# Performance work log

Measured on AMD Instinct MI355X. Metric: run time of the kernel, lower is better.

The kernel has to match this reference:

```python
import jax, jax.numpy as jnp
import numpy as np

B, KEY, D, U, MODES = 16384, 64, 128, 128, 32

def setup_inputs() -> dict:
    key = jax.random.key(0)
    k1, k2, k3, k4, k5 = jax.random.split(key, 5)
    return {
        "key": jax.random.normal(k1, (B, KEY), dtype=jnp.float32),
        "x": jax.random.normal(k2, (B, D), dtype=jnp.float32),
        "sens": jnp.ones((MODES,), dtype=jnp.float32),
        "keys_map": jax.random.normal(k3, (MODES, KEY), dtype=jnp.float32),
        "kernels": jax.random.normal(k4, (MODES, D, U), dtype=jnp.float32) * 0.05,
        "biases": jax.random.normal(k5, (MODES, U), dtype=jnp.float32) * 0.05,
    }

def reference(key, x, sens, keys_map, kernels, biases):
    # key: [B, KEY]; keys_map: [MODES, KEY]
    # Euclidean distance of each key to each mode's stored key.
    dist = jnp.sqrt(jnp.sum((key[:, None, :] - keys_map[None, :, :]) ** 2, axis=-1))  # [B, MODES]
    sim = jax.nn.softmax(sens / (dist + 1.0), axis=-1)  # [B, MODES]
    modes = kernels.shape[0]
    # Original: kernel_b = mean_m(sim[b,m] * kernels[m]); out_b = x_b @ kernel_b.
    # Reordered as GEMM-per-mode + weighted combine (same math):
    out = jnp.einsum('bm,bd,mdu->bu', sim, x, kernels) / modes  # [B, U]
    out = out + (sim @ biases) / modes  # mean over modes of sim-weighted biases
    return out
```

## Files before the change

### kernel.cpp

```cpp
#include <hip/hip_runtime.h>

#define BATCH 16384
#define KEYD  64
#define DDIM  128
#define UDIM  128
#define MODES 32

typedef __attribute__((ext_vector_type(8))) short bf16x8;
typedef __attribute__((ext_vector_type(4))) float f32x4;

__device__ __forceinline__ unsigned short f2bf(float f) {
  unsigned u = __float_as_uint(f);
  unsigned r = (u + 0x7FFFu + ((u >> 16) & 1u)) >> 16;
  return (unsigned short)r;
}

__device__ __forceinline__ void gld_lds16(const void* g, void* l) {
  __builtin_amdgcn_global_load_lds(
      (const __attribute__((address_space(1))) unsigned int*)g,
      (__attribute__((address_space(3))) unsigned int*)l, 16, 0, 0);
}

__global__ __launch_bounds__(256) void prep_all(
    const float* __restrict__ key, const float* __restrict__ x,
    const float* __restrict__ sens, const float* __restrict__ keys_map,
    const float* __restrict__ kernels, const float* __restrict__ biases,
    float* __restrict__ sim, unsigned short* __restrict__ x16,
    unsigned short* __restrict__ kb16, unsigned short* __restrict__ bb16) {
  const int t = threadIdx.x;
  const int bid = blockIdx.x;

  if (bid < BATCH / 32) {
    __shared__ float kr[32][KEYD];
    *(float4*)(&kr[0][0] + t * 4) =
        *(const float4*)(key + (long)bid * 32 * KEYD + t * 4);
    *(float4*)(&kr[0][0] + 1024 + t * 4) =
        *(const float4*)(key + (long)bid * 32 * KEYD + 1024 + t * 4);

    const int lane = t & 63, wave = t >> 6;
    const int m = lane & 31, h = lane >> 5;
    float kreg[32];
    {
      const float* kmp = keys_map + m * KEYD + h * 32;
      #pragma unroll
      for (int j = 0; j < 32; j += 4) {
        const float4 v = *(const float4*)(kmp + j);
        kreg[j] = v.x; kreg[j + 1] = v.y; kreg[j + 2] = v.z; kreg[j + 3] = v.w;
      }
    }
    const float sv = sens[m];
    __syncthreads();

    #pragma unroll
    for (int rr = 0; rr < 8; ++rr) {
      const int rl = wave * 8 + rr;
      const long row = (long)bid * 32 + rl;

      float d2h = 0.f;
      #pragma unroll
      for (int j = 0; j < 32; j += 2) {
        const float2 kv = *(const float2*)(&kr[rl][h * 32 + j]);
        float a = kv.x - kreg[j], b = kv.y - kreg[j + 1];
        d2h += a * a + b * b;
      }
      float d2 = d2h + __shfl_xor(d2h, 32, 64);
      float logit = sv / (sqrtf(d2) + 1.0f);
      float mx = logit;
      #pragma unroll
      for (int off = 16; off > 0; off >>= 1) mx = fmaxf(mx, __shfl_xor(mx, off, 64));
      float e = __expf(logit - mx);
      float s = e;
      #pragma unroll
      for (int off = 16; off > 0; off >>= 1) s += __shfl_xor(s, off, 64);
      if (h == 0) sim[row * MODES + m] = e / s;

      const float2 xv = *(const float2*)(x + row * DDIM + lane * 2);
      ushort2 o; o.x = f2bf(xv.x); o.y = f2bf(xv.y);
      *(ushort2*)(x16 + row * DDIM + lane * 2) = o;
    }
  } else {
    int tt = (bid - BATCH / 32) * 256 + t;
    if (tt < MODES * 16 * UDIM) {
      int u = tt & 127, kb = (tt >> 7) & 15, m = tt >> 11;
      const float* src = kernels + (long)((m * 16 + kb) * 8) * UDIM + u;
      ushort4 lo, hi;
      lo.x = f2bf(src[0 * UDIM]); lo.y = f2bf(src[1 * UDIM]);
      lo.z = f2bf(src[2 * UDIM]); lo.w = f2bf(src[3 * UDIM]);
      hi.x = f2bf(src[4 * UDIM]); hi.y = f2bf(src[5 * UDIM]);
      hi.z = f2bf(src[6 * UDIM]); hi.w = f2bf(src[7 * UDIM]);
      *(ushort4*)(kb16 + (long)tt * 8) = lo;
      *(ushort4*)(kb16 + (long)tt * 8 + 4) = hi;
    } else {
      int tb = tt - MODES * 16 * UDIM;
      int u = tb & 127, kb = tb >> 7;
      const float* src = biases + kb * 8 * UDIM + u;
      ushort4 lo, hi;
      lo.x = f2bf(src[0 * UDIM]); lo.y = f2bf(src[1 * UDIM]);
      lo.z = f2bf(src[2 * UDIM]); lo.w = f2bf(src[3 * UDIM]);
      hi.x = f2bf(src[4 * UDIM]); hi.y = f2bf(src[5 * UDIM]);
      hi.z = f2bf(src[6 * UDIM]); hi.w = f2bf(src[7 * UDIM]);
      *(ushort4*)(bb16 + (long)tb * 8) = lo;
      *(ushort4*)(bb16 + (long)tb * 8 + 4) = hi;
    }
  }
}

__global__ __launch_bounds__(256, 2) void gemm_poly(
    const unsigned short* __restrict__ x16, const unsigned short* __restrict__ kb16,
    const unsigned short* __restrict__ bb16, const float* __restrict__ sim,
    float* __restrict__ partial) {
  __shared__ alignas(16) unsigned short bsh[2][16 * UDIM * 8];
  __shared__ alignas(16) float simT[8][128];

  const int t = threadIdx.x;
  const int lane = t & 63, w = t >> 6;
  const int q = lane >> 4, l16 = lane & 15;
  const int wrow = (w >> 1) * 64, wcol = (w & 1) * 64;
  const long bm = (long)blockIdx.x * 128;
  const int split = blockIdx.y;

  {
    int rrow = t >> 1, mg = (t & 1) * 4;
    const float4 v = *(const float4*)(sim + (bm + rrow) * MODES + split * 8 + mg);
    simT[mg + 0][rrow] = v.x; simT[mg + 1][rrow] = v.y;
    simT[mg + 2][rrow] = v.z; simT[mg + 3][rrow] = v.w;
  }

  bf16x8 aF[4][4];
  #pragma unroll
  for (int rt = 0; rt < 4; ++rt)
    #pragma unroll
    for (int ks = 0; ks < 4; ++ks)
      aF[rt][ks] = *(const bf16x8*)(x16 + (bm + wrow + rt * 16 + l16) * DDIM + ks * 32 + q * 8);

  const unsigned short* kbase = kb16 + (long)(split * 8) * (16 * UDIM * 8);
  #pragma unroll
  for (int i = 0; i < 8; ++i) {
    int off = (t + i * 256) * 8;
    gld_lds16(kbase + off, &bsh[0][off]);
  }

  f32x4 acc[4][4] = {};

  for (int mi = 0; mi < 8; ++mi) {
    __syncthreads();
    if (mi < 7) {
      const unsigned short* src = kbase + (long)(mi + 1) * (16 * UDIM * 8);
      unsigned short* dst = bsh[(mi + 1) & 1];
      #pragma unroll
      for (int i = 0; i < 8; ++i) {
        int off = (t + i * 256) * 8;
        gld_lds16(src + off, dst + off);
      }
    }

    const unsigned short* bs = bsh[mi & 1];
    bf16x8 bF[4][4];
    #pragma unroll
    for (int ks = 0; ks < 4; ++ks)
      #pragma unroll
      for (int ct = 0; ct < 4; ++ct)
        bF[ks][ct] = *(const bf16x8*)&bs[(((ks * 4 + q) * UDIM) + wcol + ct * 16 + l16) * 8];

    #pragma unroll
    for (int rt = 0; rt < 4; ++rt) {
      f32x4 tmp[4] = {};
      #pragma unroll
      for (int ks = 0; ks < 4; ++ks)
        #pragma unroll
        for (int ct = 0; ct < 4; ++ct)
          tmp[ct] = __builtin_amdgcn_mfma_f32_16x16x32_bf16(aF[rt][ks], bF[ks][ct], tmp[ct], 0, 0, 0);
      const f32x4 s = *(const f32x4*)&simT[mi][wrow + rt * 16 + q * 4];
      #pragma unroll
      for (int ct = 0; ct < 4; ++ct)
        acc[rt][ct] += s * tmp[ct];
    }
  }

  if (split == 0) {
    bf16x8 sF[4];
    #pragma unroll
    for (int rt = 0; rt < 4; ++rt) {
      const float* sp = sim + (bm + wrow + rt * 16 + l16) * MODES + q * 8;
      bf16x8 f;
      #pragma unroll
      for (int j = 0; j < 8; ++j) f[j] = (short)f2bf(sp[j]);
      sF[rt] = f;
    }
    #pragma unroll
    for (int ct = 0; ct < 4; ++ct) {
      bf16x8 bb = *(const bf16x8*)(bb16 + (long)(q * UDIM + wcol + ct * 16 + l16) * 8);
      #pragma unroll
      for (int rt = 0; rt < 4; ++rt)
        acc[rt][ct] = __builtin_amdgcn_mfma_f32_16x16x32_bf16(sF[rt], bb, acc[rt][ct], 0, 0, 0);
    }
  }

  float* part = partial + (long)split * ((long)BATCH * UDIM);
  #pragma unroll
  for (int rt = 0; rt < 4; ++rt)
    #pragma unroll
    for (int ct = 0; ct < 4; ++ct) {
      long row = bm + wrow + rt * 16 + q * 4;
      int col = wcol + ct * 16 + l16;
      #pragma unroll
      for (int r = 0; r < 4; ++r)
        part[(row + r) * UDIM + col] = acc[rt][ct][r];
    }
}

__global__ __launch_bounds__(256) void reduce_parts(
    const float* __restrict__ partial, float* __restrict__ out) {
  const long i = ((long)blockIdx.x * 256 + threadIdx.x) * 4;
  const long S = (long)BATCH * UDIM;
  const f32x4 p0 = *(const f32x4*)(partial + i);
  const f32x4 p1 = *(const f32x4*)(partial + S + i);
  const f32x4 p2 = *(const f32x4*)(partial + 2 * S + i);
  const f32x4 p3 = *(const f32x4*)(partial + 3 * S + i);
  *(f32x4*)(out + i) = (p0 + p1 + p2 + p3) * (1.0f / MODES);
}

extern "C" void kernel_launch(void* const* d_in, const int* in_sizes, int n_in,
                              void* d_out, int out_size, void* d_ws, size_t ws_size,
                              hipStream_t stream) {
  const float* key      = (const float*)d_in[0];
  const float* x        = (const float*)d_in[1];
  const float* sens     = (const float*)d_in[2];
  const float* keys_map = (const float*)d_in[3];
  const float* kernels  = (const float*)d_in[4];
  const float* biases   = (const float*)d_in[5];
  float* out = (float*)d_out;

  char* ws = (char*)d_ws;
  float*          sim  = (float*)ws;
  unsigned short* x16  = (unsigned short*)(ws + (2u << 20));
  unsigned short* kb16 = (unsigned short*)(ws + (6u << 20));
  unsigned short* bb16 = (unsigned short*)(ws + (7u << 20));
  float*          part = (float*)(ws + (8u << 20));

  prep_all<<<BATCH / 32 + 258, 256, 0, stream>>>(
      key, x, sens, keys_map, kernels, biases, sim, x16, kb16, bb16);
  gemm_poly<<<dim3(BATCH / 128, 4), 256, 0, stream>>>(x16, kb16, bb16, sim, part);
  reduce_parts<<<(BATCH * UDIM) / (256 * 4), 256, 0, stream>>>(part, out);
}
```

Measured before the change: 107.9 us.

## Split GEMM output columns across blocks and drop LDS double buffering

Each GEMM block now computes a 128x64 output tile instead of 128x128, so the grid doubles to 8 in y (4 mode splits × 2 column halves). Each wave now covers 32 rows × 64 columns. The kernel-weight LDS buffer shrinks to a single 64-column buffer with no double buffering, and occupancy is raised to 3 blocks per SM. The intent is more parallelism and occupancy at the cost of loading the x fragments twice and losing the prefetch overlap, since each mode's load is now followed by a barrier.

```diff
diff --git a/kernel.cpp b/kernel.cpp
--- a/kernel.cpp
+++ b/kernel.cpp
@@ -105,19 +105,20 @@
   }
 }
 
-__global__ __launch_bounds__(256, 2) void gemm_poly(
+__global__ __launch_bounds__(256, 3) void gemm_poly(
     const unsigned short* __restrict__ x16, const unsigned short* __restrict__ kb16,
     const unsigned short* __restrict__ bb16, const float* __restrict__ sim,
     float* __restrict__ partial) {
-  __shared__ alignas(16) unsigned short bsh[2][16 * UDIM * 8];
+  __shared__ alignas(16) unsigned short bsh[16 * 64 * 8];
   __shared__ alignas(16) float simT[8][128];
 
   const int t = threadIdx.x;
   const int lane = t & 63, w = t >> 6;
   const int q = lane >> 4, l16 = lane & 15;
-  const int wrow = (w >> 1) * 64, wcol = (w & 1) * 64;
+  const int wrow = w * 32;
   const long bm = (long)blockIdx.x * 128;
-  const int split = blockIdx.y;
+  const int split = blockIdx.y & 3;
+  const int c0 = (blockIdx.y >> 2) * 64;
 
   {
     int rrow = t >> 1, mg = (t & 1) * 4;
@@ -126,44 +127,39 @@
     simT[mg + 2][rrow] = v.z; simT[mg + 3][rrow] = v.w;
   }
 
-  bf16x8 aF[4][4];
+  bf16x8 aF[2][4];
   #pragma unroll
-  for (int rt = 0; rt < 4; ++rt)
+  for (int rt = 0; rt < 2; ++rt)
     #pragma unroll
     for (int ks = 0; ks < 4; ++ks)
       aF[rt][ks] = *(const bf16x8*)(x16 + (bm + wrow + rt * 16 + l16) * DDIM + ks * 32 + q * 8);
 
-  const unsigned short* kbase = kb16 + (long)(split * 8) * (16 * UDIM * 8);
-  #pragma unroll
-  for (int i = 0; i < 8; ++i) {
-    int off = (t + i * 256) * 8;
-    gld_lds16(kbase + off, &bsh[0][off]);
-  }
-
-  f32x4 acc[4][4] = {};
+  f32x4 acc[2][4] = {};
 
   for (int mi = 0; mi < 8; ++mi) {
+    const int m = split * 8 + mi;
     __syncthreads();
-    if (mi < 7) {
-      const unsigned short* src = kbase + (long)(mi + 1) * (16 * UDIM * 8);
-      unsigned short* dst = bsh[(mi + 1) & 1];
-      #pragma unroll
-      for (int i = 0; i < 8; ++i) {
-        int off = (t + i * 256) * 8;
-        gld_lds16(src + off, dst + off);
+    {
+      const unsigned short* msrc = kb16 + (long)m * (16 * UDIM * 8) + c0 * 8;
+      #pragma unroll
+      for (int i = 0; i < 4; ++i) {
+        int e = (t + i * 256) * 8;
+        int kblk = e >> 9, within = e & 511;
+        gld_lds16(msrc + (long)kblk * (UDIM * 8) + within,
+                  (unsigned short*)bsh + e);
       }
     }
-
-    const unsigned short* bs = bsh[mi & 1];
+    __syncthreads();
+
     bf16x8 bF[4][4];
     #pragma unroll
     for (int ks = 0; ks < 4; ++ks)
       #pragma unroll
       for (int ct = 0; ct < 4; ++ct)
-        bF[ks][ct] = *(const bf16x8*)&bs[(((ks * 4 + q) * UDIM) + wcol + ct * 16 + l16) * 8];
-
-    #pragma unroll
-    for (int rt = 0; rt < 4; ++rt) {
+        bF[ks][ct] = *(const bf16x8*)&bsh[(((ks * 4 + q) * 64) + ct * 16 + l16) * 8];
+
+    #pragma unroll
+    for (int rt = 0; rt < 2; ++rt) {
       f32x4 tmp[4] = {};
       #pragma unroll
       for (int ks = 0; ks < 4; ++ks)
@@ -178,9 +174,9 @@
   }
 
   if (split == 0) {
-    bf16x8 sF[4];
-    #pragma unroll
-    for (int rt = 0; rt < 4; ++rt) {
+    bf16x8 sF[2];
+    #pragma unroll
+    for (int rt = 0; rt < 2; ++rt) {
       const float* sp = sim + (bm + wrow + rt * 16 + l16) * MODES + q * 8;
       bf16x8 f;
       #pragma unroll
@@ -189,20 +185,20 @@
     }
     #pragma unroll
     for (int ct = 0; ct < 4; ++ct) {
-      bf16x8 bb = *(const bf16x8*)(bb16 + (long)(q * UDIM + wcol + ct * 16 + l16) * 8);
-      #pragma unroll
-      for (int rt = 0; rt < 4; ++rt)
+      bf16x8 bb = *(const bf16x8*)(bb16 + (long)(q * UDIM + c0 + ct * 16 + l16) * 8);
+      #pragma unroll
+      for (int rt = 0; rt < 2; ++rt)
         acc[rt][ct] = __builtin_amdgcn_mfma_f32_16x16x32_bf16(sF[rt], bb, acc[rt][ct], 0, 0, 0);
     }
   }
 
   float* part = partial + (long)split * ((long)BATCH * UDIM);
   #pragma unroll
-  for (int rt = 0; rt < 4; ++rt)
+  for (int rt = 0; rt < 2; ++rt)
     #pragma unroll
     for (int ct = 0; ct < 4; ++ct) {
       long row = bm + wrow + rt * 16 + q * 4;
-      int col = wcol + ct * 16 + l16;
+      int col = c0 + ct * 16 + l16;
       #pragma unroll
       for (int r = 0; r < 4; ++r)
         part[(row + r) * UDIM + col] = acc[rt][ct][r];
@@ -240,6 +236,6 @@
 
   prep_all<<<BATCH / 32 + 258, 256, 0, stream>>>(
       key, x, sens, keys_map, kernels, biases, sim, x16, kb16, bb16);
-  gemm_poly<<<dim3(BATCH / 128, 4), 256, 0, stream>>>(x16, kb16, bb16, sim, part);
+  gemm_poly<<<dim3(BATCH / 128, 8), 256, 0, stream>>>(x16, kb16, bb16, sim, part);
   reduce_parts<<<(BATCH * UDIM) / (256 * 4), 256, 0, stream>>>(part, out);
 }
```

Result: slower. 110.4 us (+2.3%).

## Fuse x bf16 conversion into GEMM and fold split-K reduction via atomic counter

Applied to the files above, without the earlier changes.

Drops the x16 bf16 staging buffer: the GEMM now loads fp32 x directly and converts it to bf16 fragments in registers. The separate reduce kernel is removed. Each GEMM block bumps a per-row-tile atomic counter (zeroed by an extra prep block), and the last of the four split blocks sums the partials and writes the output. This saves a kernel launch plus a write and re-read of the converted x, at the cost of each split block reading x in fp32 (4x redundant) and a serialized tail reduction in the last-arriving block.

```diff
diff --git a/kernel.cpp b/kernel.cpp
--- a/kernel.cpp
+++ b/kernel.cpp
@@ -22,11 +22,11 @@
 }
 
 __global__ __launch_bounds__(256) void prep_all(
-    const float* __restrict__ key, const float* __restrict__ x,
-    const float* __restrict__ sens, const float* __restrict__ keys_map,
-    const float* __restrict__ kernels, const float* __restrict__ biases,
-    float* __restrict__ sim, unsigned short* __restrict__ x16,
-    unsigned short* __restrict__ kb16, unsigned short* __restrict__ bb16) {
+    const float* __restrict__ key, const float* __restrict__ sens,
+    const float* __restrict__ keys_map, const float* __restrict__ kernels,
+    const float* __restrict__ biases, float* __restrict__ sim,
+    unsigned short* __restrict__ kb16, unsigned short* __restrict__ bb16,
+    int* __restrict__ cnt) {
   const int t = threadIdx.x;
   const int bid = blockIdx.x;
 
@@ -73,12 +73,8 @@
       #pragma unroll
       for (int off = 16; off > 0; off >>= 1) s += __shfl_xor(s, off, 64);
       if (h == 0) sim[row * MODES + m] = e / s;
-
-      const float2 xv = *(const float2*)(x + row * DDIM + lane * 2);
-      ushort2 o; o.x = f2bf(xv.x); o.y = f2bf(xv.y);
-      *(ushort2*)(x16 + row * DDIM + lane * 2) = o;
-    }
-  } else {
+    }
+  } else if (bid < BATCH / 32 + 258) {
     int tt = (bid - BATCH / 32) * 256 + t;
     if (tt < MODES * 16 * UDIM) {
       int u = tt & 127, kb = (tt >> 7) & 15, m = tt >> 11;
@@ -102,15 +98,19 @@
       *(ushort4*)(bb16 + (long)tb * 8) = lo;
       *(ushort4*)(bb16 + (long)tb * 8 + 4) = hi;
     }
+  } else {
+    if (t < BATCH / 128) cnt[t] = 0;
   }
 }
 
 __global__ __launch_bounds__(256, 2) void gemm_poly(
-    const unsigned short* __restrict__ x16, const unsigned short* __restrict__ kb16,
+    const float* __restrict__ x, const unsigned short* __restrict__ kb16,
     const unsigned short* __restrict__ bb16, const float* __restrict__ sim,
-    float* __restrict__ partial) {
+    float* __restrict__ partial, int* __restrict__ cnt,
+    float* __restrict__ out) {
   __shared__ alignas(16) unsigned short bsh[2][16 * UDIM * 8];
   __shared__ alignas(16) float simT[8][128];
+  __shared__ int sOld;
 
   const int t = threadIdx.x;
   const int lane = t & 63, w = t >> 6;
@@ -130,8 +130,17 @@
   #pragma unroll
   for (int rt = 0; rt < 4; ++rt)
     #pragma unroll
-    for (int ks = 0; ks < 4; ++ks)
-      aF[rt][ks] = *(const bf16x8*)(x16 + (bm + wrow + rt * 16 + l16) * DDIM + ks * 32 + q * 8);
+    for (int ks = 0; ks < 4; ++ks) {
+      const float* xp = x + (bm + wrow + rt * 16 + l16) * DDIM + ks * 32 + q * 8;
+      const float4 lo = *(const float4*)xp;
+      const float4 hi = *(const float4*)(xp + 4);
+      bf16x8 f;
+      f[0] = (short)f2bf(lo.x); f[1] = (short)f2bf(lo.y);
+      f[2] = (short)f2bf(lo.z); f[3] = (short)f2bf(lo.w);
+      f[4] = (short)f2bf(hi.x); f[5] = (short)f2bf(hi.y);
+      f[6] = (short)f2bf(hi.z); f[7] = (short)f2bf(hi.w);
+      aF[rt][ks] = f;
+    }
 
   const unsigned short* kbase = kb16 + (long)(split * 8) * (16 * UDIM * 8);
   #pragma unroll
@@ -196,7 +205,8 @@
     }
   }
 
-  float* part = partial + (long)split * ((long)BATCH * UDIM);
+  const long S = (long)BATCH * UDIM;
+  float* part = partial + (long)split * S;
   #pragma unroll
   for (int rt = 0; rt < 4; ++rt)
     #pragma unroll
@@ -207,17 +217,24 @@
       for (int r = 0; r < 4; ++r)
         part[(row + r) * UDIM + col] = acc[rt][ct][r];
     }
-}
-
-__global__ __launch_bounds__(256) void reduce_parts(
-    const float* __restrict__ partial, float* __restrict__ out) {
-  const long i = ((long)blockIdx.x * 256 + threadIdx.x) * 4;
-  const long S = (long)BATCH * UDIM;
-  const f32x4 p0 = *(const f32x4*)(partial + i);
-  const f32x4 p1 = *(const f32x4*)(partial + S + i);
-  const f32x4 p2 = *(const f32x4*)(partial + 2 * S + i);
-  const f32x4 p3 = *(const f32x4*)(partial + 3 * S + i);
-  *(f32x4*)(out + i) = (p0 + p1 + p2 + p3) * (1.0f / MODES);
+
+  __threadfence();
+  if (t == 0) sOld = atomicAdd(&cnt[blockIdx.x], 1);
+  __syncthreads();
+  if (sOld == 3) {
+    __threadfence();
+    const f32x4* p0 = (const f32x4*)partial;
+    const f32x4* p1 = (const f32x4*)(partial + S);
+    const f32x4* p2 = (const f32x4*)(partial + 2 * S);
+    const f32x4* p3 = (const f32x4*)(partial + 3 * S);
+    f32x4* o4 = (f32x4*)out;
+    const long base = bm * UDIM / 4;
+    #pragma unroll
+    for (int i = 0; i < 16; ++i) {
+      long idx = base + i * 256 + t;
+      o4[idx] = (p0[idx] + p1[idx] + p2[idx] + p3[idx]) * (1.0f / MODES);
+    }
+  }
 }
 
 extern "C" void kernel_launch(void* const* d_in, const int* in_sizes, int n_in,
@@ -233,13 +250,13 @@
 
   char* ws = (char*)d_ws;
   float*          sim  = (float*)ws;
-  unsigned short* x16  = (unsigned short*)(ws + (2u << 20));
-  unsigned short* kb16 = (unsigned short*)(ws + (6u << 20));
-  unsigned short* bb16 = (unsigned short*)(ws + (7u << 20));
-  float*          part = (float*)(ws + (8u << 20));
-
-  prep_all<<<BATCH / 32 + 258, 256, 0, stream>>>(
-      key, x, sens, keys_map, kernels, biases, sim, x16, kb16, bb16);
-  gemm_poly<<<dim3(BATCH / 128, 4), 256, 0, stream>>>(x16, kb16, bb16, sim, part);
-  reduce_parts<<<(BATCH * UDIM) / (256 * 4), 256, 0, stream>>>(part, out);
-}
+  unsigned short* kb16 = (unsigned short*)(ws + (2u << 20));
+  unsigned short* bb16 = (unsigned short*)(ws + (3u << 20));
+  int*            cnt  = (int*)(ws + (3u << 20) + (512u << 10));
+  float*          part = (float*)(ws + (4u << 20));
+
+  prep_all<<<BATCH / 32 + 259, 256, 0, stream>>>(
+      key, sens, keys_map, kernels, biases, sim, kb16, bb16, cnt);
+  gemm_poly<<<dim3(BATCH / 128, 4), 256, 0, stream>>>(
+      x, kb16, bb16, sim, part, cnt, out);
+}
```

After: 191.2 us. 77.2% more time.

## Load B fragments directly from global into registers, drop LDS staging

Applied to the files above, without the earlier changes.

Replaces the LDS double-buffered staging of the per-mode bf16 kernel tiles with direct global-to-register loads into two register buffers (ping-pong), removing per-iteration __syncthreads and LDS reads. It also drops the occupancy hint of 2 from launch bounds and fully unrolls the mode loop. The aim is to cut LDS traffic and barrier stalls, at the cost of higher register pressure (two 4x4 bf16x8 B buffers plus A and accumulators) and redundant global/L2 reads, since each wave now fetches its own B slice.

```diff
diff --git a/kernel.cpp b/kernel.cpp
--- a/kernel.cpp
+++ b/kernel.cpp
@@ -13,12 +13,6 @@
   unsigned u = __float_as_uint(f);
   unsigned r = (u + 0x7FFFu + ((u >> 16) & 1u)) >> 16;
   return (unsigned short)r;
-}
-
-__device__ __forceinline__ void gld_lds16(const void* g, void* l) {
-  __builtin_amdgcn_global_load_lds(
-      (const __attribute__((address_space(1))) unsigned int*)g,
-      (__attribute__((address_space(3))) unsigned int*)l, 16, 0, 0);
 }
 
 __global__ __launch_bounds__(256) void prep_all(
@@ -105,11 +99,20 @@
   }
 }
 
-__global__ __launch_bounds__(256, 2) void gemm_poly(
+__device__ __forceinline__ void loadB(bf16x8 (&bF)[4][4],
+                                      const unsigned short* __restrict__ mb,
+                                      int q, int wcol, int l16) {
+  #pragma unroll
+  for (int ks = 0; ks < 4; ++ks)
+    #pragma unroll
+    for (int ct = 0; ct < 4; ++ct)
+      bF[ks][ct] = *(const bf16x8*)(mb + ((ks * 4 + q) * UDIM + wcol + ct * 16 + l16) * 8);
+}
+
+__global__ __launch_bounds__(256) void gemm_poly(
     const unsigned short* __restrict__ x16, const unsigned short* __restrict__ kb16,
     const unsigned short* __restrict__ bb16, const float* __restrict__ sim,
     float* __restrict__ partial) {
-  __shared__ alignas(16) unsigned short bsh[2][16 * UDIM * 8];
   __shared__ alignas(16) float simT[8][128];
 
   const int t = threadIdx.x;
@@ -119,48 +122,35 @@
   const long bm = (long)blockIdx.x * 128;
   const int split = blockIdx.y;
 
+  bf16x8 aF[4][4];
+  #pragma unroll
+  for (int rt = 0; rt < 4; ++rt)
+    #pragma unroll
+    for (int ks = 0; ks < 4; ++ks)
+      aF[rt][ks] = *(const bf16x8*)(x16 + (bm + wrow + rt * 16 + l16) * DDIM + ks * 32 + q * 8);
+
   {
     int rrow = t >> 1, mg = (t & 1) * 4;
     const float4 v = *(const float4*)(sim + (bm + rrow) * MODES + split * 8 + mg);
     simT[mg + 0][rrow] = v.x; simT[mg + 1][rrow] = v.y;
     simT[mg + 2][rrow] = v.z; simT[mg + 3][rrow] = v.w;
   }
-
-  bf16x8 aF[4][4];
-  #pragma unroll
-  for (int rt = 0; rt < 4; ++rt)
-    #pragma unroll
-    for (int ks = 0; ks < 4; ++ks)
-      aF[rt][ks] = *(const bf16x8*)(x16 + (bm + wrow + rt * 16 + l16) * DDIM + ks * 32 + q * 8);
+  __syncthreads();
 
   const unsigned short* kbase = kb16 + (long)(split * 8) * (16 * UDIM * 8);
-  #pragma unroll
-  for (int i = 0; i < 8; ++i) {
-    int off = (t + i * 256) * 8;
-    gld_lds16(kbase + off, &bsh[0][off]);
-  }
+
+  bf16x8 bA[4][4], bB[4][4];
+  loadB(bA, kbase, q, wcol, l16);
 
   f32x4 acc[4][4] = {};
 
+  #pragma unroll
   for (int mi = 0; mi < 8; ++mi) {
-    __syncthreads();
     if (mi < 7) {
-      const unsigned short* src = kbase + (long)(mi + 1) * (16 * UDIM * 8);
-      unsigned short* dst = bsh[(mi + 1) & 1];
-      #pragma unroll
-      for (int i = 0; i < 8; ++i) {
-        int off = (t + i * 256) * 8;
-        gld_lds16(src + off, dst + off);
-      }
-    }
-
-    const unsigned short* bs = bsh[mi & 1];
-    bf16x8 bF[4][4];
-    #pragma unroll
-    for (int ks = 0; ks < 4; ++ks)
-      #pragma unroll
-      for (int ct = 0; ct < 4; ++ct)
-        bF[ks][ct] = *(const bf16x8*)&bs[(((ks * 4 + q) * UDIM) + wcol + ct * 16 + l16) * 8];
+      if (mi & 1) loadB(bA, kbase + (long)(mi + 1) * (16 * UDIM * 8), q, wcol, l16);
+      else        loadB(bB, kbase + (long)(mi + 1) * (16 * UDIM * 8), q, wcol, l16);
+    }
+    const bf16x8 (&bF)[4][4] = (mi & 1) ? bB : bA;
 
     #pragma unroll
     for (int rt = 0; rt < 4; ++rt) {
```

New measurement: 111.7 us. 3.5% more time.
